# Kernel tuning notes

Measured on AMD Instinct MI355X. Metric: run time of the kernel, lower is better.

The kernel has to match this reference:

```python
import jax, jax.numpy as jnp
import numpy as np

EMB = 1024
HEADS = 16
FFN = 4096
EPS = 1e-5


def _layernorm(x, g, b):
    mu = jnp.mean(x, axis=-1, keepdims=True)
    var = jnp.mean((x - mu) ** 2, axis=-1, keepdims=True)
    return (x - mu) * jax.lax.rsqrt(var + EPS) * g + b


def setup_inputs() -> dict:
    key = jax.random.key(0)
    ks = jax.random.split(key, 8)
    B, T = 2, 2048
    s_in = 1.0 / np.sqrt(EMB)
    s_ffn = 1.0 / np.sqrt(FFN)
    return {
        "x": jax.random.normal(ks[0], (B, T, EMB), jnp.float32),
        "positions": jnp.arange(B * T, dtype=jnp.int64 if jax.config.jax_enable_x64 else jnp.int32).reshape(B, T),
        "ln1_g": jnp.ones((EMB,), jnp.float32),
        "ln1_b": jnp.zeros((EMB,), jnp.float32),
        "ln2_g": jnp.ones((EMB,), jnp.float32),
        "ln2_b": jnp.zeros((EMB,), jnp.float32),
        "Wq": jax.random.normal(ks[1], (EMB, EMB), jnp.float32) * s_in,
        "bq": jnp.zeros((EMB,), jnp.float32),
        "Wk": jax.random.normal(ks[2], (EMB, EMB), jnp.float32) * s_in,
        "bk": jnp.zeros((EMB,), jnp.float32),
        "Wv": jax.random.normal(ks[3], (EMB, EMB), jnp.float32) * s_in,
        "bv": jnp.zeros((EMB,), jnp.float32),
        "Wo": jax.random.normal(ks[4], (EMB, EMB), jnp.float32) * s_in,
        "bo": jnp.zeros((EMB,), jnp.float32),
        "W1": jax.random.normal(ks[5], (EMB, FFN), jnp.float32) * s_in,
        "b1": jnp.zeros((FFN,), jnp.float32),
        "W2": jax.random.normal(ks[6], (FFN, EMB), jnp.float32) * s_ffn,
        "b2": jnp.zeros((EMB,), jnp.float32),
    }


def reference(x, positions, ln1_g, ln1_b, ln2_g, ln2_b,
              Wq, bq, Wk, bk, Wv, bv, Wo, bo, W1, b1, W2, b2):
    B, T, C = x.shape
    H, D = HEADS, C // HEADS
    # x = ln1(x); then residual branches add onto the normalized x (as in source)
    x = _layernorm(x, ln1_g, ln1_b)
    # --- self attention (rope=None, mask=None, dropout inactive) ---
    q = (x @ Wq + bq).reshape(B, T, H, D).transpose(0, 2, 1, 3)  # [B,H,T,D]
    k = (x @ Wk + bk).reshape(B, T, H, D).transpose(0, 2, 1, 3)
    v = (x @ Wv + bv).reshape(B, T, H, D).transpose(0, 2, 1, 3)
    scale = 1.0 / jnp.sqrt(jnp.asarray(D, x.dtype))
    attn = jnp.einsum("bhtd,bhsd->bhts", q, k) * scale  # [B,H,T,T]
    attn = jax.nn.softmax(attn, axis=-1)
    attn_out = jnp.einsum("bhts,bhsd->bhtd", attn, v)
    attn_out = attn_out.transpose(0, 2, 1, 3).reshape(B, T, C)
    attn_out = attn_out @ Wo + bo
    x = x + attn_out
    # --- FFN with exact (erf) GELU, matching torch nn.GELU default ---
    h = _layernorm(x, ln2_g, ln2_b)
    h = jax.nn.gelu(h @ W1 + b1, approximate=False)
    h = h @ W2 + b2
    return x + h
```

## Files before the change

kernel.cpp:

```cpp
#include <hip/hip_runtime.h>
#include <cstdint>
#include <cstddef>

typedef __bf16 bf16;
typedef __bf16 bf16x8 __attribute__((ext_vector_type(8)));
typedef __bf16 bf16x4 __attribute__((ext_vector_type(4)));
typedef float f32x4 __attribute__((ext_vector_type(4)));
typedef float f32x16 __attribute__((ext_vector_type(16)));

#define TOKENS 4096
#define TSEQ   2048
#define NHEADS 16
#define HDIM   64
#define CDIM   1024

typedef __attribute__((address_space(3))) unsigned int lds_uint;
typedef __attribute__((address_space(1))) const unsigned int g_uint;
__device__ __forceinline__ void glds16(const bf16* g, bf16* l) {
  __builtin_amdgcn_global_load_lds((g_uint*)g, (lds_uint*)l, 16, 0, 0);
}

__device__ __forceinline__ float gelu_f(float v) {
  float g2 = v * (1.5957691216f + 0.0713548163f * v * v);
  return v / (1.0f + __expf(-g2));
}

#define NBUF 17
struct DetectArgs { const void* p[NBUF]; int n[NBUF]; };

__global__ __launch_bounds__(256) void detect_kernel(DetectArgs a, int* __restrict__ flags) {
  __shared__ int s_nz, s_bl;
  if (threadIdx.x == 0) { s_nz = 0; s_bl = 0; }
  __syncthreads();
  int i = blockIdx.x;
  const unsigned int* w = (const unsigned int*)a.p[i];
  int nwords = a.n[i] / 2; if (nwords > 2048) nwords = 2048;
  int nz = 0, bl = 0;
  for (int j = threadIdx.x; j < nwords; j += 256) {
    unsigned int v = w[j];
    if (v != 0u) {
      nz++;
      unsigned int e = (v >> 7) & 0xFFu;
      if (e >= 100u && e <= 140u) bl++;
    }
  }
  atomicAdd(&s_nz, nz);
  atomicAdd(&s_bl, bl);
  __syncthreads();
  if (threadIdx.x == 0) flags[i] = (2 * s_bl >= s_nz) ? 1 : 0;
}

__device__ __forceinline__ float ld_any(const void* p, size_t idx, bool isb) {
  return isb ? (float)((const bf16*)p)[idx] : ((const float*)p)[idx];
}

__device__ __forceinline__ void ln_stats(float s, float s2, int tid, float& mu, float& rstd) {
#pragma unroll
  for (int off = 32; off; off >>= 1) {
    s  += __shfl_down(s, off);
    s2 += __shfl_down(s2, off);
  }
  __shared__ float red[8];
  int w = tid >> 6;
  if ((tid & 63) == 0) { red[w] = s; red[4 + w] = s2; }
  __syncthreads();
  if (tid == 0) {
    red[0] = red[0] + red[1] + red[2] + red[3];
    red[4] = red[4] + red[5] + red[6] + red[7];
  }
  __syncthreads();
  mu = red[0] * (1.0f / CDIM);
  float var = fmaxf(red[4] * (1.0f / CDIM) - mu * mu, 0.f);
  rstd = rsqrtf(var + 1e-5f);
}

__global__ __launch_bounds__(256) void ln_f32(const float* __restrict__ x,
                                              const bf16* __restrict__ g,
                                              const bf16* __restrict__ b,
                                              bf16* __restrict__ y) {
  int row = blockIdx.x, tid = threadIdx.x;
  float v[4]; float s = 0.f, s2 = 0.f;
#pragma unroll
  for (int i = 0; i < 4; i++) {
    float f = x[(size_t)row * CDIM + tid * 4 + i];
    v[i] = f; s += f; s2 += f * f;
  }
  float mu, rstd;
  ln_stats(s, s2, tid, mu, rstd);
  bf16* yr = y + (size_t)row * CDIM;
#pragma unroll
  for (int i = 0; i < 4; i++) {
    int c = tid * 4 + i;
    yr[c] = (bf16)((v[i] - mu) * rstd * (float)g[c] + (float)b[c]);
  }
}

struct MegaArgs {
  const void* w_in[6]; bf16* w_out[6]; int wK[6], wN[6], wflag[6];
  const void* vp[10]; bf16* vd[10]; int vn[10], vfi[10];
  const void* x; const void* graw; const void* braw; bf16* y;
};

__global__ __launch_bounds__(256) void mega_pre(MegaArgs a, const int* __restrict__ flags) {
  int bid = blockIdx.x;
  int tx = threadIdx.x, ty = threadIdx.y;
  int tid = tx + ty * 64;
  if (bid < 3072) {
    __shared__ bf16 tile[64][65];
    int mi, start;
    if (bid < 1024)      { mi = bid >> 8; start = mi << 8; }
    else if (bid < 2048) { mi = 4; start = 1024; }
    else                 { mi = 5; start = 2048; }
    int tb = bid - start;
    int nT = a.wN[mi] >> 6;
    int kb = (tb / nT) * 64, nb = (tb % nT) * 64;
    int K = a.wK[mi], N = a.wN[mi];
    bool isb = flags[a.wflag[mi]] != 0;
    const void* in = a.w_in[mi]; bf16* out = a.w_out[mi];
    for (int i = ty; i < 64; i += 4)
      tile[i][tx] = (bf16)ld_any(in, (size_t)(kb + i) * N + nb + tx, isb);
    __syncthreads();
    for (int i = ty; i < 64; i += 4)
      out[(size_t)(nb + i) * K + kb + tx] = tile[tx][i];
  } else if (bid == 3072) {
    for (int i = 0; i < 10; i++) {
      bool isb = flags[a.vfi[i]] != 0;
      const void* in = a.vp[i]; bf16* out = a.vd[i]; int n = a.vn[i];
      for (int j = tid; j < n; j += 256)
        out[j] = (bf16)ld_any(in, j, isb);
    }
  } else {
    int row = bid - 3073;
    bool isb  = flags[0] != 0;
    bool gisb = flags[1] != 0;
    bool bisb = flags[2] != 0;
    float v[4]; float s = 0.f, s2 = 0.f;
#pragma unroll
    for (int i = 0; i < 4; i++) {
      float f = ld_any(a.x, (size_t)row * CDIM + tid * 4 + i, isb);
      v[i] = f; s += f; s2 += f * f;
    }
    float mu, rstd;
    ln_stats(s, s2, tid, mu, rstd);
    bf16* yr = a.y + (size_t)row * CDIM;
#pragma unroll
    for (int i = 0; i < 4; i++) {
      int c = tid * 4 + i;
      float gv = ld_any(a.graw, c, gisb);
      float bv = ld_any(a.braw, c, bisb);
      yr[c] = (bf16)((v[i] - mu) * rstd * gv + bv);
    }
  }
}

template <int BM, int BN>
__device__ __forceinline__ void gemm_core(const bf16* __restrict__ A,
                                          const bf16* __restrict__ Bt,
                                          int K, int m0, int n0,
                                          bf16* As, bf16* Bs,
                                          f32x4 (&acc)[BM / 32][BN / 32]) {
  constexpr int SI = BM / 32, SJ = BN / 32;
  int t = threadIdx.x;
  int wave = t >> 6, lane = t & 63, quad = lane >> 4, l16 = lane & 15;
  int wm = (wave & 1) * (BM / 2), wn = (wave >> 1) * (BN / 2);
  int srow = t >> 2, sc = t & 3;
  int swz = (srow >> 1) & 3;
  const bf16* ga[BM / 64];
  const bf16* gb[BN / 64];
#pragma unroll
  for (int h = 0; h < BM / 64; h++)
    ga[h] = A + (size_t)(m0 + h * 64 + srow) * K + (sc ^ swz) * 8;
#pragma unroll
  for (int h = 0; h < BN / 64; h++)
    gb[h] = Bt + (size_t)(n0 + h * 64 + srow) * K + (sc ^ swz) * 8;

  for (int k0 = 0; k0 < K; k0 += 64) {
#pragma unroll
    for (int q = 0; q < 2; q++) {
#pragma unroll
      for (int h = 0; h < BM / 64; h++)
        glds16(ga[h] + k0 + q * 32, As + q * (BM * 32) + h * 2048 + srow * 32 + sc * 8);
#pragma unroll
      for (int h = 0; h < BN / 64; h++)
        glds16(gb[h] + k0 + q * 32, Bs + q * (BN * 32) + h * 2048 + srow * 32 + sc * 8);
    }
    __syncthreads();
#pragma unroll
    for (int q = 0; q < 2; q++) {
      bf16x8 af[SI], bfr[SJ];
#pragma unroll
      for (int i = 0; i < SI; i++) {
        int m = wm + i * 16 + l16;
        af[i] = *(const bf16x8*)&As[q * (BM * 32) + m * 32 + ((quad ^ ((m >> 1) & 3)) * 8)];
      }
#pragma unroll
      for (int j = 0; j < SJ; j++) {
        int n = wn + j * 16 + l16;
        bfr[j] = *(const bf16x8*)&Bs[q * (BN * 32) + n * 32 + ((quad ^ ((n >> 1) & 3)) * 8)];
      }
#pragma unroll
      for (int i = 0; i < SI; i++)
#pragma unroll
        for (int j = 0; j < SJ; j++)
          acc[i][j] = __builtin_amdgcn_mfma_f32_16x16x32_bf16(af[i], bfr[j], acc[i][j], 0, 0, 0);
    }
    __syncthreads();
  }
}

#define EPI_NONE 0
#define EPI_RES  1
#define EPI_GELU 2

template <int BM, int BN, int EPI, typename OutT, typename ResT>
__global__ __launch_bounds__(256) void gemm128(const bf16* __restrict__ A,
                                               const bf16* __restrict__ Bt,
                                               const bf16* __restrict__ bias,
                                               const ResT* __restrict__ res,
                                               OutT* __restrict__ C,
                                               int N, int K) {
  __shared__ alignas(16) bf16 As[2 * BM * 32];
  __shared__ alignas(16) bf16 Bs[2 * BN * 32];
  int m0 = blockIdx.y * BM, n0 = blockIdx.x * BN;
  f32x4 acc[BM / 32][BN / 32] = {};
  gemm_core<BM, BN>(A, Bt, K, m0, n0, As, Bs, acc);

  int t = threadIdx.x, wave = t >> 6, lane = t & 63, quad = lane >> 4, l16 = lane & 15;
  int wm = (wave & 1) * (BM / 2), wn = (wave >> 1) * (BN / 2);
#pragma unroll
  for (int i = 0; i < BM / 32; i++)
#pragma unroll
    for (int j = 0; j < BN / 32; j++) {
      int n = n0 + wn + j * 16 + l16;
      float bv = (float)bias[n];
#pragma unroll
      for (int r = 0; r < 4; r++) {
        int m = m0 + wm + i * 16 + quad * 4 + r;
        float v = acc[i][j][r] + bv;
        if (EPI == EPI_GELU)      v = gelu_f(v);
        else if (EPI == EPI_RES)  v += (float)res[(size_t)m * N + n];
        C[(size_t)m * N + n] = (OutT)v;
      }
    }
}

__device__ __forceinline__ void gemm256_core(const bf16* __restrict__ A,
                                             const bf16* __restrict__ Bt,
                                             int K, int m0, int n0,
                                             bf16* sm, f32x4 (&acc)[8][4]) {
  const int NT = K >> 6;
  const int t = threadIdx.x;
  const int lane = t & 63, quad = lane >> 4, l16 = lane & 15;
  const int wave = t >> 6;
  const int wm = (wave & 1) * 128, wn = (wave >> 1) * 64;
  const int srow = t >> 2, sc = t & 3;
  const int swz = (srow >> 1) & 3;
  const int rA = (srow & 63) + ((srow >> 6) << 7);
  const bf16* gA = A + (size_t)(m0 + rA) * K + ((sc ^ swz) << 3);
  const bf16* gB = Bt + (size_t)(n0 + srow) * K + ((sc ^ swz) << 3);
  const int ldsA = rA * 32 + sc * 8;
  const int ldsB = srow * 32 + sc * 8;

  auto stA = [&](int tile, int u) {
    if (tile >= NT) return;
    const bf16* g = gA + (size_t)(u << 6) * K + (tile << 6);
    bf16* l = sm + ((tile & 1) << 15) + ldsA + (u << 11);
    glds16(g, l);
    glds16(g + 32, l + 8192);
  };
  auto stB = [&](int tile, int h) {
    if (tile >= NT) return;
    const bf16* g = gB + (size_t)(h << 7) * K + (tile << 6);
    bf16* l = sm + ((tile & 1) << 15) + 16384 + ldsB + (h << 12);
    glds16(g, l);
    glds16(g + 32, l + 8192);
  };

  stB(0, 0); stB(0, 1); stA(0, 0); stA(0, 1);
  stB(1, 0); stB(1, 1); stA(1, 0);
  asm volatile("s_waitcnt vmcnt(6)" ::: "memory");
  __builtin_amdgcn_s_barrier();
  asm volatile("" ::: "memory");

  bf16x8 bfr[2][4];

#define LDB256(buf)                                                        \
  _Pragma("unroll") for (int q = 0; q < 2; q++)                            \
  _Pragma("unroll") for (int j = 0; j < 4; j++) {                          \
    int nl = wn + j * 16 + l16;                                            \
    bfr[q][j] = *(const bf16x8*)&sm[((buf) << 15) + 16384 + q * 8192 +     \
                                    nl * 32 + ((quad ^ ((nl >> 1) & 3)) << 3)]; \
  }

#define PHASE256(buf, P, STAGE, EXTRAWAIT)                                 \
  {                                                                        \
    bf16x8 af[2][2];                                                       \
    _Pragma("unroll") for (int q = 0; q < 2; q++)                          \
    _Pragma("unroll") for (int i2 = 0; i2 < 2; i2++) {                     \
      int ml = wm + (P) * 32 + i2 * 16 + l16;                              \
      af[q][i2] = *(const bf16x8*)&sm[((buf) << 15) + q * 8192 + ml * 32 + \
                                      ((quad ^ ((ml >> 1) & 3)) << 3)];    \
    }                                                                      \
    if ((P) == 0) { LDB256(buf); }                                         \
    STAGE;                                                                 \
    asm volatile("" ::: "memory");                                         \
    __builtin_amdgcn_s_barrier();                                          \
    asm volatile("s_waitcnt lgkmcnt(0)" ::: "memory");                     \
    __builtin_amdgcn_s_setprio(1);                                         \
    _Pragma("unroll") for (int q = 0; q < 2; q++)                          \
    _Pragma("unroll") for (int i2 = 0; i2 < 2; i2++)                       \
    _Pragma("unroll") for (int j = 0; j < 4; j++)                          \
      acc[(P) * 2 + i2][j] = __builtin_amdgcn_mfma_f32_16x16x32_bf16(      \
          af[q][i2], bfr[q][j], acc[(P) * 2 + i2][j], 0, 0, 0);            \
    __builtin_amdgcn_s_setprio(0);                                         \
    asm volatile("" ::: "memory");                                         \
    EXTRAWAIT;                                                             \
    __builtin_amdgcn_s_barrier();                                          \
    asm volatile("" ::: "memory");                                         \
  }

  for (int t0 = 0; t0 < NT; t0 += 2) {
    const int t1 = t0 + 1;
    PHASE256(0, 0, stA(t1, 1), (void)0);
    PHASE256(0, 1, stB(t0 + 2, 0), (void)0);
    PHASE256(0, 2, stB(t0 + 2, 1), (void)0);
    PHASE256(0, 3, stA(t0 + 2, 0),
             asm volatile("s_waitcnt vmcnt(6)" ::: "memory"));
    PHASE256(1, 0, stA(t0 + 2, 1), (void)0);
    PHASE256(1, 1, stB(t1 + 2, 0), (void)0);
    PHASE256(1, 2, stB(t1 + 2, 1), (void)0);
    PHASE256(1, 3, stA(t1 + 2, 0),
             asm volatile("s_waitcnt vmcnt(6)" ::: "memory"));
  }
#undef PHASE256
#undef LDB256
}

__device__ __forceinline__ void xcd_swizzle(int& bx, int& by) {
  int gx = gridDim.x;
  int nwg = gx * gridDim.y;
  int bid = blockIdx.x + blockIdx.y * gx;
  int wg = (bid & 7) * (nwg >> 3) + (bid >> 3);
  bx = wg % gx; by = wg / gx;
}

__global__ __launch_bounds__(512, 2) void gemm256_gelu(const bf16* __restrict__ A,
                                                       const bf16* __restrict__ Bt,
                                                       const bf16* __restrict__ bias,
                                                       bf16* __restrict__ C,
                                                       int N, int K) {
  __shared__ alignas(16) bf16 sm[65536];
  int bx, by; xcd_swizzle(bx, by);
  int m0 = by * 256, n0 = bx * 256;
  f32x4 acc[8][4] = {};
  gemm256_core(A, Bt, K, m0, n0, sm, acc);

  int t = threadIdx.x, wave = t >> 6, lane = t & 63, quad = lane >> 4, l16 = lane & 15;
  int wm = (wave & 1) * 128, wn = (wave >> 1) * 64;
#pragma unroll
  for (int i = 0; i < 8; i++)
#pragma unroll
    for (int j = 0; j < 4; j++) {
      int n = n0 + wn + j * 16 + l16;
      float bv = (float)bias[n];
#pragma unroll
      for (int r = 0; r < 4; r++) {
        int m = m0 + wm + i * 16 + quad * 4 + r;
        C[(size_t)m * N + n] = (bf16)gelu_f(acc[i][j][r] + bv);
      }
    }
}

__global__ __launch_bounds__(512, 2) void gemm256_qkv(const bf16* __restrict__ A,
                                                      const bf16* __restrict__ Bt,
                                                      const bf16* __restrict__ bias,
                                                      bf16* __restrict__ QK,
                                                      bf16* __restrict__ Vt) {
  __shared__ alignas(16) bf16 sm[65536];
  int bx, by; xcd_swizzle(bx, by);
  int m0 = by * 256, n0 = bx * 256;
  f32x4 acc[8][4] = {};
  gemm256_core(A, Bt, 1024, m0, n0, sm, acc);

  int t = threadIdx.x, wave = t >> 6, lane = t & 63, quad = lane >> 4, l16 = lane & 15;
  int wm = (wave & 1) * 128, wn = (wave >> 1) * 64;
#pragma unroll
  for (int i = 0; i < 8; i++)
#pragma unroll
    for (int j = 0; j < 4; j++) {
      int n = n0 + wn + j * 16 + l16;
      float bv = (float)bias[n];
      int mb = m0 + wm + i * 16 + quad * 4;
      if (n < 1024) {
#pragma unroll
        for (int r = 0; r < 4; r++)
          QK[(size_t)(mb + r) * 2048 + n] = (bf16)((acc[i][j][r] + bv) * 0.18033688011112042f);
      } else if (n < 2048) {
#pragma unroll
        for (int r = 0; r < 4; r++)
          QK[(size_t)(mb + r) * 2048 + n] = (bf16)(acc[i][j][r] + bv);
      } else {
        bf16x4 pk;
#pragma unroll
        for (int r = 0; r < 4; r++) pk[r] = (bf16)(acc[i][j][r] + bv);
        *(bf16x4*)&Vt[(size_t)(n - 2048) * TOKENS + mb] = pk;
      }
    }
}

__global__ __launch_bounds__(256, 2) void attn_kernel(const bf16* __restrict__ QK,
                                                      const bf16* __restrict__ Vt,
                                                      bf16* __restrict__ O) {
  __shared__ alignas(16) bf16 Ks[2][4096];
  __shared__ alignas(16) bf16 Vs[2][4096];
  int bid = blockIdx.x;
  int xcd = bid & 7, slot = bid >> 3;
  int g = xcd + 8 * (slot >> 4);
  int q0 = (slot & 15) * 128;
  int h = g & 15, b = g >> 4;
  int t = threadIdx.x, wave = t >> 6, lane = t & 63;
  int l31 = lane & 31, l5 = lane >> 5, l7 = lane & 7;

  const bf16* Qg = QK;
  const bf16* Kg = QK + 1024;
  const size_t bT = (size_t)b * TSEQ;
  const int h64 = h * 64;

  int sr = lane >> 3;
  int sch = l7 ^ sr;
  auto stage = [&](int tile, int buf) {
    size_t krow = bT + tile * 64 + wave * 8 + sr;
    bf16* kd = &Ks[buf][wave * 512 + lane * 8];
    glds16(&Kg[krow * 2048 + h64 + sch * 8], kd);
    glds16(&Kg[(krow + 32) * 2048 + h64 + sch * 8], kd + 2048);
    size_t vrow = (size_t)(h64 + wave * 8 + sr) * TOKENS + bT + tile * 64 + sch * 8;
    bf16* vd = &Vs[buf][wave * 512 + lane * 8];
    glds16(&Vt[vrow], vd);
    glds16(&Vt[vrow + (size_t)32 * TOKENS], vd + 2048);
  };

  bf16x8 qf[4];
  {
    size_t qrow = bT + q0 + wave * 32 + l31;
    const bf16* qp = &Qg[qrow * 2048 + h64 + l5 * 8];
#pragma unroll
    for (int ds = 0; ds < 4; ds++) qf[ds] = *(const bf16x8*)(qp + ds * 16);
  }

  f32x16 accO0 = {}, accO1 = {}, accL = {};
  const bf16 one = (bf16)1.0f;
  const bf16x8 onesv = {one, one, one, one, one, one, one, one};

  auto vread = [&](const bf16* VsC, int d, int w) -> bf16x8 {
    union { struct { bf16x4 lo, hi; } p; bf16x8 v; } u;
    u.p.lo = *(const bf16x4*)&VsC[d * 64 + (((2 * w) ^ l7) * 8) + 4 * l5];
    u.p.hi = *(const bf16x4*)&VsC[d * 64 + (((2 * w + 1) ^ l7) * 8) + 4 * l5];
    return u.v;
  };

  stage(0, 0);
  __syncthreads();

  for (int it = 0; it < TSEQ / 64; it++) {
    int cur = it & 1;
    if (it + 1 < TSEQ / 64) stage(it + 1, cur ^ 1);

    const bf16* KsC = &Ks[cur][0];
    const bf16* VsC = &Vs[cur][0];

    f32x16 st0 = {}, st1 = {};
#pragma unroll
    for (int ds = 0; ds < 4; ds++) {
      int chs = ((ds * 2 + l5) ^ l7) * 8;
      bf16x8 k0 = *(const bf16x8*)&KsC[l31 * 64 + chs];
      bf16x8 k1 = *(const bf16x8*)&KsC[(32 + l31) * 64 + chs];
      st0 = __builtin_amdgcn_mfma_f32_32x32x16_bf16(k0, qf[ds], st0, 0, 0, 0);
      st1 = __builtin_amdgcn_mfma_f32_32x32x16_bf16(k1, qf[ds], st1, 0, 0, 0);
    }

    bf16x8 pa[4];
#pragma unroll
    for (int j = 0; j < 8; j++) {
      pa[0][j] = (bf16)exp2f(fminf(st0[j], 86.f));
      pa[1][j] = (bf16)exp2f(fminf(st0[8 + j], 86.f));
      pa[2][j] = (bf16)exp2f(fminf(st1[j], 86.f));
      pa[3][j] = (bf16)exp2f(fminf(st1[8 + j], 86.f));
    }

#pragma unroll
    for (int w = 0; w < 4; w++) {
      bf16x8 v0 = vread(VsC, l31, w);
      bf16x8 v1 = vread(VsC, 32 + l31, w);
      accO0 = __builtin_amdgcn_mfma_f32_32x32x16_bf16(pa[w], v0, accO0, 0, 0, 0);
      accO1 = __builtin_amdgcn_mfma_f32_32x32x16_bf16(pa[w], v1, accO1, 0, 0, 0);
      accL  = __builtin_amdgcn_mfma_f32_32x32x16_bf16(pa[w], onesv, accL, 0, 0, 0);
    }

    __syncthreads();
  }

#pragma unroll
  for (int r = 0; r < 16; r++) {
    int q = (r & 3) + 8 * (r >> 2) + 4 * l5;
    float rl = 1.0f / fmaxf(accL[r], 1e-30f);
    size_t orow = (bT + q0 + wave * 32 + q) * CDIM + h64;
    O[orow + l31]      = (bf16)(accO0[r] * rl);
    O[orow + 32 + l31] = (bf16)(accO1[r] * rl);
  }
}

extern "C" void kernel_launch(void* const* d_in, const int* in_sizes, int n_in,
                              void* d_out, int out_size, void* d_ws, size_t ws_size,
                              hipStream_t stream) {
  char* ws = (char*)d_ws;
  const size_t MB = 1024 * 1024;
  const size_t KB = 1024;

  int* flags = (int*)ws;
  bf16* vec_c = (bf16*)(ws + 4 * KB);
  bf16* ln1g_c = vec_c + 0 * 8192;
  bf16* ln1b_c = vec_c + 1 * 8192;
  bf16* ln2g_c = vec_c + 2 * 8192;
  bf16* ln2b_c = vec_c + 3 * 8192;
  bf16* bqkv_c = vec_c + 4 * 8192;
  bf16* bo_c   = vec_c + 6 * 8192;
  bf16* b1_c   = vec_c + 7 * 8192;
  bf16* b2_c   = vec_c + 8 * 8192;

  bf16*  WqkvT  = (bf16*)(ws + 1 * MB);
  bf16*  WoT    = (bf16*)(ws + 7 * MB);
  bf16*  W1T    = (bf16*)(ws + 9 * MB);
  bf16*  W2T    = (bf16*)(ws + 17 * MB);
  bf16*  xn     = (bf16*)(ws + 25 * MB);
  bf16*  QKbuf  = (bf16*)(ws + 33 * MB);
  bf16*  Vtbuf  = (bf16*)(ws + 49 * MB);
  bf16*  ab     = (bf16*)(ws + 57 * MB);
  float* xmid32 = (float*)(ws + 65 * MB);
  bf16*  h2     = (bf16*)(ws + 81 * MB);
  bf16*  f1     = (bf16*)(ws + 33 * MB);

  const int din_idx[NBUF] = {0, 2, 3, 4, 5, 6, 7, 8, 9, 10, 11, 12, 13, 14, 15, 16, 17};
  DetectArgs da;
  for (int i = 0; i < NBUF; i++) { da.p[i] = d_in[din_idx[i]]; da.n[i] = in_sizes[din_idx[i]]; }
  detect_kernel<<<NBUF, 256, 0, stream>>>(da, flags);

  MegaArgs ma;
  {
    const void* wi[6] = {d_in[6], d_in[8], d_in[10], d_in[12], d_in[14], d_in[16]};
    bf16* wo[6] = {WqkvT, WqkvT + 1024 * 1024, WqkvT + 2 * 1024 * 1024, WoT, W1T, W2T};
    const int wK[6] = {1024, 1024, 1024, 1024, 1024, 4096};
    const int wN[6] = {1024, 1024, 1024, 1024, 4096, 1024};
    const int wf[6] = {5, 7, 9, 11, 13, 15};
    for (int i = 0; i < 6; i++) {
      ma.w_in[i] = wi[i]; ma.w_out[i] = wo[i];
      ma.wK[i] = wK[i]; ma.wN[i] = wN[i]; ma.wflag[i] = wf[i];
    }
    const int vf[10] = {1, 2, 3, 4, 6, 8, 10, 12, 14, 16};
    bf16* vd[10] = {ln1g_c, ln1b_c, ln2g_c, ln2b_c,
                    bqkv_c, bqkv_c + 1024, bqkv_c + 2048, bo_c, b1_c, b2_c};
    for (int i = 0; i < 10; i++) {
      int di = din_idx[vf[i]];
      ma.vp[i] = d_in[di]; ma.vd[i] = vd[i]; ma.vn[i] = in_sizes[di]; ma.vfi[i] = vf[i];
    }
    ma.x = d_in[0]; ma.graw = d_in[2]; ma.braw = d_in[3]; ma.y = xn;
  }
  mega_pre<<<3072 + 1 + TOKENS, dim3(64, 4), 0, stream>>>(ma, flags);

  gemm256_qkv<<<dim3(12, 16), 512, 0, stream>>>(xn, WqkvT, bqkv_c, QKbuf, Vtbuf);

  attn_kernel<<<512, 256, 0, stream>>>(QKbuf, Vtbuf, ab);

  gemm128<64, 128, EPI_RES, float, bf16><<<dim3(8, 64), 256, 0, stream>>>(
      ab, WoT, bo_c, xn, xmid32, 1024, 1024);

  ln_f32<<<TOKENS, 256, 0, stream>>>(xmid32, ln2g_c, ln2b_c, h2);

  gemm256_gelu<<<dim3(16, 16), 512, 0, stream>>>(h2, W1T, b1_c, f1, 4096, 1024);

  gemm128<64, 128, EPI_RES, float, float><<<dim3(8, 64), 256, 0, stream>>>(
      f1, W2T, b2_c, xmid32, (float*)d_out, 1024, 4096);
}
```

Before: 393.1 us.

## Split-K the W2 GEMM and deepen attention K/V pipelining with permuted V layout

```diff
diff --git a/kernel.cpp b/kernel.cpp
--- a/kernel.cpp
+++ b/kernel.cpp
@@ -246,7 +246,7 @@
 
 __device__ __forceinline__ void gemm256_core(const bf16* __restrict__ A,
                                              const bf16* __restrict__ Bt,
-                                             int K, int m0, int n0,
+                                             int K, int lda, int ldb, int m0, int n0,
                                              bf16* sm, f32x4 (&acc)[8][4]) {
   const int NT = K >> 6;
   const int t = threadIdx.x;
@@ -256,21 +256,21 @@
   const int srow = t >> 2, sc = t & 3;
   const int swz = (srow >> 1) & 3;
   const int rA = (srow & 63) + ((srow >> 6) << 7);
-  const bf16* gA = A + (size_t)(m0 + rA) * K + ((sc ^ swz) << 3);
-  const bf16* gB = Bt + (size_t)(n0 + srow) * K + ((sc ^ swz) << 3);
+  const bf16* gA = A + (size_t)(m0 + rA) * lda + ((sc ^ swz) << 3);
+  const bf16* gB = Bt + (size_t)(n0 + srow) * ldb + ((sc ^ swz) << 3);
   const int ldsA = rA * 32 + sc * 8;
   const int ldsB = srow * 32 + sc * 8;
 
   auto stA = [&](int tile, int u) {
     if (tile >= NT) return;
-    const bf16* g = gA + (size_t)(u << 6) * K + (tile << 6);
+    const bf16* g = gA + (size_t)(u << 6) * lda + (tile << 6);
     bf16* l = sm + ((tile & 1) << 15) + ldsA + (u << 11);
     glds16(g, l);
     glds16(g + 32, l + 8192);
   };
   auto stB = [&](int tile, int h) {
     if (tile >= NT) return;
-    const bf16* g = gB + (size_t)(h << 7) * K + (tile << 6);
+    const bf16* g = gB + (size_t)(h << 7) * ldb + (tile << 6);
     bf16* l = sm + ((tile & 1) << 15) + 16384 + ldsB + (h << 12);
     glds16(g, l);
     glds16(g + 32, l + 8192);
@@ -353,7 +353,7 @@
   int bx, by; xcd_swizzle(bx, by);
   int m0 = by * 256, n0 = bx * 256;
   f32x4 acc[8][4] = {};
-  gemm256_core(A, Bt, K, m0, n0, sm, acc);
+  gemm256_core(A, Bt, K, K, K, m0, n0, sm, acc);
 
   int t = threadIdx.x, wave = t >> 6, lane = t & 63, quad = lane >> 4, l16 = lane & 15;
   int wm = (wave & 1) * 128, wn = (wave >> 1) * 64;
@@ -369,6 +369,52 @@
         C[(size_t)m * N + n] = (bf16)gelu_f(acc[i][j][r] + bv);
       }
     }
+}
+
+__global__ __launch_bounds__(512, 2) void gemm256_part(const bf16* __restrict__ A,
+                                                       const bf16* __restrict__ Bt,
+                                                       bf16* __restrict__ P0, bf16* __restrict__ P1,
+                                                       bf16* __restrict__ P2, bf16* __restrict__ P3,
+                                                       int lda) {
+  __shared__ alignas(16) bf16 sm[65536];
+  int m0 = blockIdx.y * 256, n0 = blockIdx.x * 256, kz = blockIdx.z;
+  const bf16* Ak = A + (size_t)kz * 1024;
+  const bf16* Bk = Bt + (size_t)kz * 1024;
+  f32x4 acc[8][4] = {};
+  gemm256_core(Ak, Bk, 1024, lda, lda, m0, n0, sm, acc);
+
+  bf16* P = (kz == 0) ? P0 : (kz == 1) ? P1 : (kz == 2) ? P2 : P3;
+  int t = threadIdx.x, wave = t >> 6, lane = t & 63, quad = lane >> 4, l16 = lane & 15;
+  int wm = (wave & 1) * 128, wn = (wave >> 1) * 64;
+#pragma unroll
+  for (int i = 0; i < 8; i++)
+#pragma unroll
+    for (int j = 0; j < 4; j++) {
+      int n = n0 + wn + j * 16 + l16;
+#pragma unroll
+      for (int r = 0; r < 4; r++) {
+        int m = m0 + wm + i * 16 + quad * 4 + r;
+        P[(size_t)m * 1024 + n] = (bf16)acc[i][j][r];
+      }
+    }
+}
+
+__global__ __launch_bounds__(256) void w2_reduce(const bf16* __restrict__ P0, const bf16* __restrict__ P1,
+                                                 const bf16* __restrict__ P2, const bf16* __restrict__ P3,
+                                                 const float* __restrict__ res, const bf16* __restrict__ bias,
+                                                 float* __restrict__ out) {
+  int c = threadIdx.x * 4;
+  size_t base = (size_t)blockIdx.x * 1024 + c;
+  bf16x4 a0 = *(const bf16x4*)&P0[base];
+  bf16x4 a1 = *(const bf16x4*)&P1[base];
+  bf16x4 a2 = *(const bf16x4*)&P2[base];
+  bf16x4 a3 = *(const bf16x4*)&P3[base];
+  f32x4 rv = *(const f32x4*)&res[base];
+  f32x4 o;
+#pragma unroll
+  for (int i = 0; i < 4; i++)
+    o[i] = ((float)a0[i] + (float)a1[i]) + ((float)a2[i] + (float)a3[i]) + rv[i] + (float)bias[c + i];
+  *(f32x4*)&out[base] = o;
 }
 
 __global__ __launch_bounds__(512, 2) void gemm256_qkv(const bf16* __restrict__ A,
@@ -380,7 +426,7 @@
   int bx, by; xcd_swizzle(bx, by);
   int m0 = by * 256, n0 = bx * 256;
   f32x4 acc[8][4] = {};
-  gemm256_core(A, Bt, 1024, m0, n0, sm, acc);
+  gemm256_core(A, Bt, 1024, 1024, 1024, m0, n0, sm, acc);
 
   int t = threadIdx.x, wave = t >> 6, lane = t & 63, quad = lane >> 4, l16 = lane & 15;
   int wm = (wave & 1) * 128, wn = (wave >> 1) * 64;
@@ -400,10 +446,13 @@
         for (int r = 0; r < 4; r++)
           QK[(size_t)(mb + r) * 2048 + n] = (bf16)(acc[i][j][r] + bv);
       } else {
+        int qt = (mb >> 2) & 3;
+        int qt2 = ((qt & 1) << 1) | (qt >> 1);
+        int mb2 = (mb & ~15) | (qt2 << 2);
         bf16x4 pk;
 #pragma unroll
         for (int r = 0; r < 4; r++) pk[r] = (bf16)(acc[i][j][r] + bv);
-        *(bf16x4*)&Vt[(size_t)(n - 2048) * TOKENS + mb] = pk;
+        *(bf16x4*)&Vt[(size_t)(n - 2048) * TOKENS + mb2] = pk;
       }
     }
 }
@@ -411,8 +460,7 @@
 __global__ __launch_bounds__(256, 2) void attn_kernel(const bf16* __restrict__ QK,
                                                       const bf16* __restrict__ Vt,
                                                       bf16* __restrict__ O) {
-  __shared__ alignas(16) bf16 Ks[2][4096];
-  __shared__ alignas(16) bf16 Vs[2][4096];
+  __shared__ alignas(16) bf16 KV[4][8192];
   int bid = blockIdx.x;
   int xcd = bid & 7, slot = bid >> 3;
   int g = xcd + 8 * (slot >> 4);
@@ -430,13 +478,12 @@
   int sch = l7 ^ sr;
   auto stage = [&](int tile, int buf) {
     size_t krow = bT + tile * 64 + wave * 8 + sr;
-    bf16* kd = &Ks[buf][wave * 512 + lane * 8];
+    bf16* kd = &KV[buf][wave * 512 + lane * 8];
     glds16(&Kg[krow * 2048 + h64 + sch * 8], kd);
     glds16(&Kg[(krow + 32) * 2048 + h64 + sch * 8], kd + 2048);
     size_t vrow = (size_t)(h64 + wave * 8 + sr) * TOKENS + bT + tile * 64 + sch * 8;
-    bf16* vd = &Vs[buf][wave * 512 + lane * 8];
-    glds16(&Vt[vrow], vd);
-    glds16(&Vt[vrow + (size_t)32 * TOKENS], vd + 2048);
+    glds16(&Vt[vrow], kd + 4096);
+    glds16(&Vt[vrow + (size_t)32 * TOKENS], kd + 6144);
   };
 
   bf16x8 qf[4];
@@ -447,56 +494,65 @@
     for (int ds = 0; ds < 4; ds++) qf[ds] = *(const bf16x8*)(qp + ds * 16);
   }
 
+  int off[4];
+#pragma unroll
+  for (int w = 0; w < 4; w++) off[w] = l31 * 64 + (((w * 2 + l5) ^ l7) * 8);
+
   f32x16 accO0 = {}, accO1 = {}, accL = {};
   const bf16 one = (bf16)1.0f;
   const bf16x8 onesv = {one, one, one, one, one, one, one, one};
 
-  auto vread = [&](const bf16* VsC, int d, int w) -> bf16x8 {
-    union { struct { bf16x4 lo, hi; } p; bf16x8 v; } u;
-    u.p.lo = *(const bf16x4*)&VsC[d * 64 + (((2 * w) ^ l7) * 8) + 4 * l5];
-    u.p.hi = *(const bf16x4*)&VsC[d * 64 + (((2 * w + 1) ^ l7) * 8) + 4 * l5];
-    return u.v;
-  };
-
   stage(0, 0);
-  __syncthreads();
-
-  for (int it = 0; it < TSEQ / 64; it++) {
-    int cur = it & 1;
-    if (it + 1 < TSEQ / 64) stage(it + 1, cur ^ 1);
-
-    const bf16* KsC = &Ks[cur][0];
-    const bf16* VsC = &Vs[cur][0];
-
-    f32x16 st0 = {}, st1 = {};
-#pragma unroll
-    for (int ds = 0; ds < 4; ds++) {
-      int chs = ((ds * 2 + l5) ^ l7) * 8;
-      bf16x8 k0 = *(const bf16x8*)&KsC[l31 * 64 + chs];
-      bf16x8 k1 = *(const bf16x8*)&KsC[(32 + l31) * 64 + chs];
-      st0 = __builtin_amdgcn_mfma_f32_32x32x16_bf16(k0, qf[ds], st0, 0, 0, 0);
-      st1 = __builtin_amdgcn_mfma_f32_32x32x16_bf16(k1, qf[ds], st1, 0, 0, 0);
-    }
-
-    bf16x8 pa[4];
-#pragma unroll
-    for (int j = 0; j < 8; j++) {
-      pa[0][j] = (bf16)exp2f(fminf(st0[j], 86.f));
-      pa[1][j] = (bf16)exp2f(fminf(st0[8 + j], 86.f));
-      pa[2][j] = (bf16)exp2f(fminf(st1[j], 86.f));
-      pa[3][j] = (bf16)exp2f(fminf(st1[8 + j], 86.f));
-    }
-
-#pragma unroll
-    for (int w = 0; w < 4; w++) {
-      bf16x8 v0 = vread(VsC, l31, w);
-      bf16x8 v1 = vread(VsC, 32 + l31, w);
-      accO0 = __builtin_amdgcn_mfma_f32_32x32x16_bf16(pa[w], v0, accO0, 0, 0, 0);
-      accO1 = __builtin_amdgcn_mfma_f32_32x32x16_bf16(pa[w], v1, accO1, 0, 0, 0);
-      accL  = __builtin_amdgcn_mfma_f32_32x32x16_bf16(pa[w], onesv, accL, 0, 0, 0);
-    }
-
-    __syncthreads();
+  stage(1, 1);
+  asm volatile("s_waitcnt vmcnt(4)" ::: "memory");
+  __builtin_amdgcn_s_barrier();
+  asm volatile("" ::: "memory");
+
+  for (int it4 = 0; it4 < TSEQ / 64; it4 += 4) {
+#pragma unroll
+    for (int u = 0; u < 4; u++) {
+      int it = it4 + u;
+      if (it + 2 < TSEQ / 64) stage(it + 2, (it + 2) & 3);
+      const bf16* KB = &KV[u][0];
+
+      f32x16 st0 = {}, st1 = {};
+      __builtin_amdgcn_s_setprio(1);
+#pragma unroll
+      for (int ds = 0; ds < 4; ds++) {
+        bf16x8 k0 = *(const bf16x8*)&KB[off[ds]];
+        bf16x8 k1 = *(const bf16x8*)&KB[off[ds] + 2048];
+        st0 = __builtin_amdgcn_mfma_f32_32x32x16_bf16(k0, qf[ds], st0, 0, 0, 0);
+        st1 = __builtin_amdgcn_mfma_f32_32x32x16_bf16(k1, qf[ds], st1, 0, 0, 0);
+      }
+      __builtin_amdgcn_s_setprio(0);
+
+      bf16x8 pa[4];
+#pragma unroll
+      for (int j = 0; j < 8; j++) {
+        pa[0][j] = (bf16)exp2f(fminf(st0[j], 86.f));
+        pa[1][j] = (bf16)exp2f(fminf(st0[8 + j], 86.f));
+        pa[2][j] = (bf16)exp2f(fminf(st1[j], 86.f));
+        pa[3][j] = (bf16)exp2f(fminf(st1[8 + j], 86.f));
+      }
+
+      __builtin_amdgcn_s_setprio(1);
+#pragma unroll
+      for (int w = 0; w < 4; w++) {
+        bf16x8 v0 = *(const bf16x8*)&KB[off[w] + 4096];
+        bf16x8 v1 = *(const bf16x8*)&KB[off[w] + 6144];
+        accO0 = __builtin_amdgcn_mfma_f32_32x32x16_bf16(pa[w], v0, accO0, 0, 0, 0);
+        accO1 = __builtin_amdgcn_mfma_f32_32x32x16_bf16(pa[w], v1, accO1, 0, 0, 0);
+        accL  = __builtin_amdgcn_mfma_f32_32x32x16_bf16(pa[w], onesv, accL, 0, 0, 0);
+      }
+      __builtin_amdgcn_s_setprio(0);
+
+      if (it + 2 < TSEQ / 64)
+        asm volatile("s_waitcnt vmcnt(4)" ::: "memory");
+      else
+        asm volatile("s_waitcnt vmcnt(0)" ::: "memory");
+      __builtin_amdgcn_s_barrier();
+      asm volatile("" ::: "memory");
+    }
   }
 
 #pragma unroll
@@ -538,6 +594,10 @@
   float* xmid32 = (float*)(ws + 65 * MB);
   bf16*  h2     = (bf16*)(ws + 81 * MB);
   bf16*  f1     = (bf16*)(ws + 33 * MB);
+  bf16*  pk0    = (bf16*)(ws + 49 * MB);
+  bf16*  pk1    = (bf16*)(ws + 57 * MB);
+  bf16*  pk2    = (bf16*)(ws + 1 * MB);
+  bf16*  pk3    = (bf16*)(ws + 9 * MB);
 
   const int din_idx[NBUF] = {0, 2, 3, 4, 5, 6, 7, 8, 9, 10, 11, 12, 13, 14, 15, 16, 17};
   DetectArgs da;
@@ -577,6 +637,6 @@
 
   gemm256_gelu<<<dim3(16, 16), 512, 0, stream>>>(h2, W1T, b1_c, f1, 4096, 1024);
 
-  gemm128<64, 128, EPI_RES, float, float><<<dim3(8, 64), 256, 0, stream>>>(
-      f1, W2T, b2_c, xmid32, (float*)d_out, 1024, 4096);
-}
+  gemm256_part<<<dim3(4, 16, 4), 512, 0, stream>>>(f1, W2T, pk0, pk1, pk2, pk3, 4096);
+  w2_reduce<<<TOKENS, 256, 0, stream>>>(pk0, pk1, pk2, pk3, xmid32, b2_c, (float*)d_out);
+}
```

After: 364.7 us. 1.08x faster.
